# Optimization experiments

Hardware: AMD Instinct MI355X
Metric: run time of the kernel (lower is better)

The kernel has to match this reference:

```python
import jax, jax.numpy as jnp
import numpy as np

D_MODEL = 1024
NUM_HEADS = 16
D_K = D_MODEL // NUM_HEADS
NEG_INF = -1e9


def setup_inputs() -> dict:
    key = jax.random.key(0)
    ks = jax.random.split(key, 9)
    B, S, D = 4, 2048, D_MODEL
    scale = 1.0 / np.sqrt(D)
    inp = {
        "x": jax.random.normal(ks[0], (B, S, D), dtype=jnp.float32),
        "Wq": jax.random.normal(ks[1], (D, D), dtype=jnp.float32) * scale,
        "bq": jnp.zeros((D,), dtype=jnp.float32),
        "Wk": jax.random.normal(ks[2], (D, D), dtype=jnp.float32) * scale,
        "bk": jnp.zeros((D,), dtype=jnp.float32),
        "Wv": jax.random.normal(ks[3], (D, D), dtype=jnp.float32) * scale,
        "bv": jnp.zeros((D,), dtype=jnp.float32),
        "Wo": jax.random.normal(ks[4], (D, D), dtype=jnp.float32) * scale,
        "bo": jnp.zeros((D,), dtype=jnp.float32),
    }
    return inp


def reference(x, Wq, bq, Wk, bk, Wv, bv, Wo, bo):
    B, S, D = x.shape
    H, dk = NUM_HEADS, D_K
    # padding mask: token is pad if any feature == 0; shape [B,1,1,S] (keys)
    mask = (x == 0).any(axis=-1)[:, None, None, :]

    def split_heads(t):  # [B,S,D] -> [B,H,S,dk]
        return t.reshape(B, S, H, dk).transpose(0, 2, 1, 3)

    q = split_heads(x @ Wq + bq)
    k = split_heads(x @ Wk + bk)
    v = split_heads(x @ Wv + bv)

    scores = jnp.einsum("bhqd,bhkd->bhqk", q, k) / np.sqrt(dk).astype(x.dtype)
    scores = jnp.where(mask, jnp.asarray(NEG_INF, x.dtype), scores)
    weights = jax.nn.softmax(scores, axis=-1)
    context = jnp.einsum("bhqk,bhkd->bhqd", weights, v)
    context = context.transpose(0, 2, 1, 3).reshape(B, S, D)
    return context @ Wo + bo
```

## Files before the change

kernel.cpp:

```cpp
#include <hip/hip_runtime.h>
#include <cstdint>
#include <cstddef>

static constexpr int Bz = 4, S = 2048, Dm = 1024, H = 16, DK = 64;
static constexpr int M = Bz * S;

typedef __attribute__((ext_vector_type(8))) short bf16x8;
typedef __attribute__((ext_vector_type(4))) float f32x4;

__device__ __forceinline__ unsigned short f2b(float f) {
    unsigned u = __float_as_uint(f);
    return (unsigned short)((u + 0x7FFFu + ((u >> 16) & 1u)) >> 16);
}

__device__ __forceinline__ unsigned cvtpk(float lo, float hi) {
    unsigned r;
    asm("v_cvt_pk_bf16_f32 %0, %1, %2" : "=v"(r) : "v"(lo), "v"(hi));
    return r;
}

__device__ __forceinline__ void gld_lds16(const void* g, void* l) {
    __builtin_amdgcn_global_load_lds(
        (const __attribute__((address_space(1))) unsigned int*)g,
        (__attribute__((address_space(3))) unsigned int*)l, 16, 0, 0);
}

__global__ __launch_bounds__(256) void k_convx(const float* __restrict__ x,
                                               unsigned short* __restrict__ xb,
                                               unsigned char* __restrict__ mask) {
    const int row = blockIdx.x;
    const int t = threadIdx.x;
    const float4 v = *(const float4*)(x + (size_t)row * Dm + t * 4);
    const bool z = (v.x == 0.f) | (v.y == 0.f) | (v.z == 0.f) | (v.w == 0.f);
    ushort4 o;
    o.x = f2b(v.x); o.y = f2b(v.y); o.z = f2b(v.z); o.w = f2b(v.w);
    *(ushort4*)(xb + (size_t)row * Dm + t * 4) = o;
    __shared__ int zf;
    if (t == 0) zf = 0;
    __syncthreads();
    if (z) zf = 1;
    __syncthreads();
    if (t == 0) mask[row] = (unsigned char)zf;
}

__global__ __launch_bounds__(256) void k_convw(const float* __restrict__ Wq, const float* __restrict__ Wk,
                                               const float* __restrict__ Wv, const float* __restrict__ Wo,
                                               unsigned short* __restrict__ Wt) {
    const float* W = (blockIdx.z == 0) ? Wq : (blockIdx.z == 1) ? Wk : (blockIdx.z == 2) ? Wv : Wo;
    unsigned short* o = Wt + (size_t)blockIdx.z * Dm * Dm;
    __shared__ float tile[32][33];
    const int k0 = blockIdx.x * 32, n0 = blockIdx.y * 32;
    const int tx = threadIdx.x, ty = threadIdx.y;
#pragma unroll
    for (int i = 0; i < 4; i++)
        tile[ty + 8 * i][tx] = W[(size_t)(k0 + ty + 8 * i) * Dm + n0 + tx];
    __syncthreads();
#pragma unroll
    for (int i = 0; i < 4; i++)
        o[(size_t)(n0 + ty + 8 * i) * Dm + k0 + tx] = f2b(tile[tx][ty + 8 * i]);
}

template <int MODE>
__global__ __launch_bounds__(256) void k_gemm(
    const unsigned short* __restrict__ A,
    const unsigned short* __restrict__ Bw,
    const float* __restrict__ bias0, const float* __restrict__ bias1, const float* __restrict__ bias2,
    unsigned short* __restrict__ Qo, unsigned short* __restrict__ Ko,
    unsigned short* __restrict__ Vto, float* __restrict__ Co)
{
    __shared__ unsigned short sA[128 * 32];
    __shared__ unsigned short sB[128 * 32];
    const int m0 = blockIdx.x * 128;
    const int gn0 = blockIdx.y * 128;
    const int tid = threadIdx.x;
    const int lane = tid & 63;
    const int wid = tid >> 6;
    const int wm = wid & 1, wn = wid >> 1;
    const int srow = tid >> 2;
    const int sc8 = (tid & 3) * 8;
    const int lr = lane & 15;
    const int lg = lane >> 4;
    f32x4 acc[4][4] = {};
    const unsigned short* Ag = A + (size_t)(m0 + srow) * Dm + sc8;
    const unsigned short* Bg = Bw + (size_t)(gn0 + srow) * Dm + sc8;
    unsigned short* const lA = sA + wid * 512;
    unsigned short* const lB = sB + wid * 512;
    for (int k0 = 0; k0 < Dm; k0 += 32) {
        __syncthreads();
        gld_lds16(Ag + k0, lA);
        gld_lds16(Ag + (size_t)64 * Dm + k0, lA + 2048);
        gld_lds16(Bg + k0, lB);
        gld_lds16(Bg + (size_t)64 * Dm + k0, lB + 2048);
        __syncthreads();
        bf16x8 af[4], bg[4];
#pragma unroll
        for (int mi = 0; mi < 4; mi++)
            af[mi] = *(const bf16x8*)&sA[(wm * 64 + mi * 16 + lr) * 32 + lg * 8];
#pragma unroll
        for (int ni = 0; ni < 4; ni++)
            bg[ni] = *(const bf16x8*)&sB[(wn * 64 + ni * 16 + lr) * 32 + lg * 8];
#pragma unroll
        for (int mi = 0; mi < 4; mi++)
#pragma unroll
            for (int ni = 0; ni < 4; ni++)
                acc[mi][ni] = __builtin_amdgcn_mfma_f32_16x16x32_bf16(af[mi], bg[ni], acc[mi][ni], 0, 0, 0);
    }
#pragma unroll
    for (int mi = 0; mi < 4; mi++) {
        const int row0 = m0 + wm * 64 + mi * 16 + lg * 4;
#pragma unroll
        for (int ni = 0; ni < 4; ni++) {
            const int gn = gn0 + wn * 64 + ni * 16 + lr;
            const int t = gn >> 10;
            const int n = gn & 1023;
            const int h = n >> 6, d = n & 63;
            const float bsv = (MODE == 0)
                ? ((t == 0) ? bias0[n] : (t == 1) ? bias1[n] : bias2[n])
                : bias0[gn];
#pragma unroll
            for (int r = 0; r < 4; r++) {
                const int row = row0 + r;
                const float v = acc[mi][ni][r] + bsv;
                if (MODE == 0) {
                    const int bb = row >> 11;
                    const int s = row & (S - 1);
                    const size_t bh = (size_t)bb * H + h;
                    const unsigned short ub = f2b(v);
                    if (t == 0)      Qo[(bh * S + s) * DK + d] = ub;
                    else if (t == 1) Ko[(bh * S + s) * DK + d] = ub;
                    else {
                        const int k5 = s & 31;
                        const int sp = (s & ~31) | ((k5 & 12) << 1) | ((k5 >> 4) << 2) | (k5 & 3);
                        Vto[(bh * DK + d) * S + sp] = ub;
                    }
                } else {
                    Co[(size_t)row * Dm + gn] = v;
                }
            }
        }
    }
}

__global__ __launch_bounds__(512) void k_attn(
    const unsigned short* __restrict__ Q, const unsigned short* __restrict__ K,
    const unsigned short* __restrict__ Vt, const unsigned char* __restrict__ mask,
    unsigned short* __restrict__ ctx)
{
    __shared__ unsigned short sK[2 * 4096];
    __shared__ unsigned short sV[2 * 4096];
    const int wg = blockIdx.x;
    const int sz = (wg & 7) * 128 + (wg >> 3);
    const int xt = sz & 15;
    const int bh = sz >> 4;
    const int bidx = bh >> 4, h = bh & 15;
    const int tid = threadIdx.x, lane = tid & 63, wid = tid >> 6;
    const int lr = lane & 15, lg = lane >> 4;
    const int qbase = xt * 128 + wid * 16;
    const size_t hoff = (size_t)bh * S * DK;
    const bf16x8 aq0 = *(const bf16x8*)(Q + hoff + (size_t)(qbase + lr) * DK + lg * 8);
    const bf16x8 aq1 = *(const bf16x8*)(Q + hoff + (size_t)(qbase + lr) * DK + 32 + lg * 8);
    const unsigned char* mrow = mask + bidx * S;
    f32x4 o[4] = {};
    f32x4 lvec = {};
    constexpr float SCL2 = 0.125f * 1.44269504089f;
    constexpr float CSH  = 8.0f * 1.44269504089f;
    const int rsub = lane >> 3;
    const int csrc = ((lane & 7) ^ rsub) << 4;
    const char* gK = (const char*)(K + hoff) + (size_t)(wid * 8 + rsub) * (DK * 2) + csrc;
    const char* gV = (const char*)(Vt + hoff) + (size_t)(wid * 8 + rsub) * (S * 2) + csrc;
    constexpr int NT = S / 64;
    unsigned short* const dK0 = sK + wid * 512;
    unsigned short* const dV0 = sV + wid * 512;
    unsigned short* const dK1 = dK0 + 4096;
    unsigned short* const dV1 = dV0 + 4096;
    const char* const sKb0 = (const char*)sK;
    const char* const sKb1 = sKb0 + 8192;
    const char* const sVb0 = (const char*)sV;
    const char* const sVb1 = sVb0 + 8192;

    gld_lds16(gK, dK0);
    gld_lds16(gV, dV0);
    unsigned char mb = mrow[lane];
    gK += 8192; gV += 128;

    auto body = [&](int t, const char* sKc, const char* sVc,
                    unsigned short* dKn, unsigned short* dVn) {
        asm volatile("s_waitcnt vmcnt(0)" ::: "memory");
        __builtin_amdgcn_s_barrier();
        __builtin_amdgcn_sched_barrier(0);
        const unsigned char mbc = mb;
        if (t + 1 < NT) {
            gld_lds16(gK, dKn);
            gld_lds16(gV, dVn);
            mb = mrow[(t + 1) * 64 + lane];
            gK += 8192; gV += 128;
        }
        const unsigned long long bal = __ballot(mbc != 0);
        f32x4 zz[4];
        __builtin_amdgcn_s_setprio(1);
#pragma unroll
        for (int nt = 0; nt < 4; nt++) {
            const int row = nt * 16 + lr;
            const int sw = (row & 7) << 4;
            const bf16x8 kf0 = *(const bf16x8*)(sKc + ((row * 128 + lg * 16) ^ sw));
            const bf16x8 kf1 = *(const bf16x8*)(sKc + ((row * 128 + 64 + lg * 16) ^ sw));
            f32x4 a = {};
            a = __builtin_amdgcn_mfma_f32_16x16x32_bf16(kf0, aq0, a, 0, 0, 0);
            zz[nt] = __builtin_amdgcn_mfma_f32_16x16x32_bf16(kf1, aq1, a, 0, 0, 0);
        }
        __builtin_amdgcn_s_setprio(0);
        if (bal) {
#pragma unroll
            for (int nt = 0; nt < 4; nt++)
#pragma unroll
                for (int r = 0; r < 4; r++)
                    if ((bal >> (nt * 16 + lg * 4 + r)) & 1) zz[nt][r] = -1e9f;
        }
#pragma unroll
        for (int nt = 0; nt < 4; nt++) {
            zz[nt] = zz[nt] * SCL2 - CSH;
#pragma unroll
            for (int r = 0; r < 4; r++) zz[nt][r] = exp2f(zz[nt][r]);
            lvec += zz[nt];
        }
        union { unsigned u[4]; bf16x8 v; } w0, w1;
        w0.u[0] = cvtpk(zz[0][0], zz[0][1]); w0.u[1] = cvtpk(zz[0][2], zz[0][3]);
        w0.u[2] = cvtpk(zz[1][0], zz[1][1]); w0.u[3] = cvtpk(zz[1][2], zz[1][3]);
        w1.u[0] = cvtpk(zz[2][0], zz[2][1]); w1.u[1] = cvtpk(zz[2][2], zz[2][3]);
        w1.u[2] = cvtpk(zz[3][0], zz[3][1]); w1.u[3] = cvtpk(zz[3][2], zz[3][3]);
        __builtin_amdgcn_s_setprio(1);
#pragma unroll
        for (int dt = 0; dt < 4; dt++) {
            const int row = dt * 16 + lr;
            const int sw = (row & 7) << 4;
            const bf16x8 v0 = *(const bf16x8*)(sVc + ((row * 128 + lg * 16) ^ sw));
            const bf16x8 v1 = *(const bf16x8*)(sVc + ((row * 128 + 64 + lg * 16) ^ sw));
            o[dt] = __builtin_amdgcn_mfma_f32_16x16x32_bf16(w0.v, v0, o[dt], 0, 0, 0);
            o[dt] = __builtin_amdgcn_mfma_f32_16x16x32_bf16(w1.v, v1, o[dt], 0, 0, 0);
        }
        __builtin_amdgcn_s_setprio(0);
        asm volatile("s_waitcnt lgkmcnt(0)" ::: "memory");
    };

    for (int t = 0; t < NT; t += 2) {
        body(t,     sKb0, sVb0, dK1, dV1);
        body(t + 1, sKb1, sVb1, dK0, dV0);
    }

    float ls = (lvec[0] + lvec[1]) + (lvec[2] + lvec[3]);
    ls += __shfl_xor(ls, 16, 64);
    ls += __shfl_xor(ls, 32, 64);
#pragma unroll
    for (int r = 0; r < 4; r++) {
        const float lq = __shfl(ls, lg * 4 + r, 16);
        const float inv = 1.f / lq;
        const int s = qbase + lg * 4 + r;
#pragma unroll
        for (int dt = 0; dt < 4; dt++)
            ctx[((size_t)bidx * S + s) * Dm + h * 64 + dt * 16 + lr] = f2b(o[dt][r] * inv);
    }
}

extern "C" void kernel_launch(void* const* d_in, const int* in_sizes, int n_in,
                              void* d_out, int out_size, void* d_ws, size_t ws_size,
                              hipStream_t stream)
{
    (void)in_sizes; (void)n_in; (void)out_size; (void)ws_size;
    const float* x  = (const float*)d_in[0];
    const float* Wq = (const float*)d_in[1];
    const float* bq = (const float*)d_in[2];
    const float* Wk = (const float*)d_in[3];
    const float* bk = (const float*)d_in[4];
    const float* Wv = (const float*)d_in[5];
    const float* bv = (const float*)d_in[6];
    const float* Wo = (const float*)d_in[7];
    const float* bo = (const float*)d_in[8];
    float* out = (float*)d_out;
    char* ws = (char*)d_ws;
    unsigned short* xb  = (unsigned short*)(ws);
    unsigned short* Wt  = (unsigned short*)(ws + ((size_t)16 << 20));
    unsigned short* Qb  = (unsigned short*)(ws + ((size_t)24 << 20));
    unsigned short* Kb  = (unsigned short*)(ws + ((size_t)40 << 20));
    unsigned short* Vtb = (unsigned short*)(ws + ((size_t)56 << 20));
    unsigned short* ctx = (unsigned short*)(ws + ((size_t)72 << 20));
    unsigned char*  msk = (unsigned char*)(ws + ((size_t)88 << 20));

    k_convx<<<dim3(M), dim3(256), 0, stream>>>(x, xb, msk);
    k_convw<<<dim3(Dm / 32, Dm / 32, 4), dim3(32, 8), 0, stream>>>(Wq, Wk, Wv, Wo, Wt);
    k_gemm<0><<<dim3(M / 128, 3072 / 128), dim3(256), 0, stream>>>(
        xb, Wt, bq, bk, bv, Qb, Kb, Vtb, nullptr);
    k_attn<<<dim3(Bz * H * (S / 128)), dim3(512), 0, stream>>>(Qb, Kb, Vtb, msk, ctx);
    k_gemm<1><<<dim3(M / 128, 1024 / 128), dim3(256), 0, stream>>>(
        ctx, Wt + (size_t)3 * Dm * Dm, bo, nullptr, nullptr, nullptr, nullptr, nullptr, out);
}
```

Baseline: 236.7 us.

## Give each attention wave two query tiles and fold softmax scale into Q

The attention kernel moves from 8 waves each owning 16 query rows to 4 waves each owning 32 rows. Each K/V fragment read from LDS now feeds twice as many MFMAs, and each wave issues two global-to-LDS loads per tile. The softmax scale (1/8 times log2 e) is folded into the Q projection epilogue, which removes the per-score multiply and the constant shift before exp2. The cost is more accumulator registers per wave (occupancy is set through launch bounds) and dropping the stabilising shift, which leaves less margin against exp2 overflow.

```diff
diff --git a/kernel.cpp b/kernel.cpp
--- a/kernel.cpp
+++ b/kernel.cpp
@@ -125,13 +125,14 @@
                     const int bb = row >> 11;
                     const int s = row & (S - 1);
                     const size_t bh = (size_t)bb * H + h;
-                    const unsigned short ub = f2b(v);
-                    if (t == 0)      Qo[(bh * S + s) * DK + d] = ub;
-                    else if (t == 1) Ko[(bh * S + s) * DK + d] = ub;
-                    else {
+                    if (t == 0) {
+                        Qo[(bh * S + s) * DK + d] = f2b(v * 0.18033688011f);
+                    } else if (t == 1) {
+                        Ko[(bh * S + s) * DK + d] = f2b(v);
+                    } else {
                         const int k5 = s & 31;
                         const int sp = (s & ~31) | ((k5 & 12) << 1) | ((k5 >> 4) << 2) | (k5 & 3);
-                        Vto[(bh * DK + d) * S + sp] = ub;
+                        Vto[(bh * DK + d) * S + sp] = f2b(v);
                     }
                 } else {
                     Co[(size_t)row * Dm + gn] = v;
@@ -141,7 +142,7 @@
     }
 }
 
-__global__ __launch_bounds__(512) void k_attn(
+__global__ __launch_bounds__(256, 4) void k_attn(
     const unsigned short* __restrict__ Q, const unsigned short* __restrict__ K,
     const unsigned short* __restrict__ Vt, const unsigned char* __restrict__ mask,
     unsigned short* __restrict__ ctx)
@@ -155,48 +156,45 @@
     const int bidx = bh >> 4, h = bh & 15;
     const int tid = threadIdx.x, lane = tid & 63, wid = tid >> 6;
     const int lr = lane & 15, lg = lane >> 4;
-    const int qbase = xt * 128 + wid * 16;
+    const int qbase = xt * 128 + wid * 32;
     const size_t hoff = (size_t)bh * S * DK;
-    const bf16x8 aq0 = *(const bf16x8*)(Q + hoff + (size_t)(qbase + lr) * DK + lg * 8);
-    const bf16x8 aq1 = *(const bf16x8*)(Q + hoff + (size_t)(qbase + lr) * DK + 32 + lg * 8);
+    const unsigned short* qp = Q + hoff + (size_t)(qbase + lr) * DK;
+    const bf16x8 aqA0 = *(const bf16x8*)(qp + lg * 8);
+    const bf16x8 aqA1 = *(const bf16x8*)(qp + 32 + lg * 8);
+    const bf16x8 aqB0 = *(const bf16x8*)(qp + 16 * DK + lg * 8);
+    const bf16x8 aqB1 = *(const bf16x8*)(qp + 16 * DK + 32 + lg * 8);
     const unsigned char* mrow = mask + bidx * S;
-    f32x4 o[4] = {};
-    f32x4 lvec = {};
-    constexpr float SCL2 = 0.125f * 1.44269504089f;
-    constexpr float CSH  = 8.0f * 1.44269504089f;
-    const int rsub = lane >> 3;
-    const int csrc = ((lane & 7) ^ rsub) << 4;
-    const char* gK = (const char*)(K + hoff) + (size_t)(wid * 8 + rsub) * (DK * 2) + csrc;
-    const char* gV = (const char*)(Vt + hoff) + (size_t)(wid * 8 + rsub) * (S * 2) + csrc;
+    f32x4 oA[4] = {}, oB[4] = {};
+    f32x4 lvA = {}, lvB = {};
+    const int rw = lane >> 3;
+    const int row0 = wid * 16 + rw;
+    const int csrc = ((lane & 7) ^ rw) << 4;
+    const char* gK0 = (const char*)(K + hoff) + (size_t)row0 * 128 + csrc;
+    const char* gK1 = gK0 + 8 * 128;
+    const char* gV0 = (const char*)(Vt + hoff) + (size_t)row0 * (S * 2) + csrc;
+    const char* gV1 = gV0 + (size_t)8 * (S * 2);
     constexpr int NT = S / 64;
-    unsigned short* const dK0 = sK + wid * 512;
-    unsigned short* const dV0 = sV + wid * 512;
-    unsigned short* const dK1 = dK0 + 4096;
-    unsigned short* const dV1 = dV0 + 4096;
-    const char* const sKb0 = (const char*)sK;
-    const char* const sKb1 = sKb0 + 8192;
-    const char* const sVb0 = (const char*)sV;
-    const char* const sVb1 = sVb0 + 8192;
-
-    gld_lds16(gK, dK0);
-    gld_lds16(gV, dV0);
+    unsigned short* const wK = sK + wid * 1024;
+    unsigned short* const wV = sV + wid * 1024;
+
+    gld_lds16(gK0, wK);        gld_lds16(gK1, wK + 512);
+    gld_lds16(gV0, wV);        gld_lds16(gV1, wV + 512);
     unsigned char mb = mrow[lane];
-    gK += 8192; gV += 128;
-
-    auto body = [&](int t, const char* sKc, const char* sVc,
-                    unsigned short* dKn, unsigned short* dVn) {
+    gK0 += 8192; gK1 += 8192; gV0 += 128; gV1 += 128;
+
+    auto body = [&](int t, const char* sKc, const char* sVc, int nbuf) {
         asm volatile("s_waitcnt vmcnt(0)" ::: "memory");
         __builtin_amdgcn_s_barrier();
         __builtin_amdgcn_sched_barrier(0);
         const unsigned char mbc = mb;
         if (t + 1 < NT) {
-            gld_lds16(gK, dKn);
-            gld_lds16(gV, dVn);
+            gld_lds16(gK0, wK + nbuf * 4096);  gld_lds16(gK1, wK + nbuf * 4096 + 512);
+            gld_lds16(gV0, wV + nbuf * 4096);  gld_lds16(gV1, wV + nbuf * 4096 + 512);
             mb = mrow[(t + 1) * 64 + lane];
-            gK += 8192; gV += 128;
+            gK0 += 8192; gK1 += 8192; gV0 += 128; gV1 += 128;
         }
         const unsigned long long bal = __ballot(mbc != 0);
-        f32x4 zz[4];
+        f32x4 zA[4], zB[4];
         __builtin_amdgcn_s_setprio(1);
 #pragma unroll
         for (int nt = 0; nt < 4; nt++) {
@@ -205,8 +203,11 @@
             const bf16x8 kf0 = *(const bf16x8*)(sKc + ((row * 128 + lg * 16) ^ sw));
             const bf16x8 kf1 = *(const bf16x8*)(sKc + ((row * 128 + 64 + lg * 16) ^ sw));
             f32x4 a = {};
-            a = __builtin_amdgcn_mfma_f32_16x16x32_bf16(kf0, aq0, a, 0, 0, 0);
-            zz[nt] = __builtin_amdgcn_mfma_f32_16x16x32_bf16(kf1, aq1, a, 0, 0, 0);
+            a = __builtin_amdgcn_mfma_f32_16x16x32_bf16(kf0, aqA0, a, 0, 0, 0);
+            zA[nt] = __builtin_amdgcn_mfma_f32_16x16x32_bf16(kf1, aqA1, a, 0, 0, 0);
+            f32x4 b = {};
+            b = __builtin_amdgcn_mfma_f32_16x16x32_bf16(kf0, aqB0, b, 0, 0, 0);
+            zB[nt] = __builtin_amdgcn_mfma_f32_16x16x32_bf16(kf1, aqB1, b, 0, 0, 0);
         }
         __builtin_amdgcn_s_setprio(0);
         if (bal) {
@@ -214,20 +215,24 @@
             for (int nt = 0; nt < 4; nt++)
 #pragma unroll
                 for (int r = 0; r < 4; r++)
-                    if ((bal >> (nt * 16 + lg * 4 + r)) & 1) zz[nt][r] = -1e9f;
+                    if ((bal >> (nt * 16 + lg * 4 + r)) & 1) { zA[nt][r] = -1e9f; zB[nt][r] = -1e9f; }
         }
 #pragma unroll
         for (int nt = 0; nt < 4; nt++) {
-            zz[nt] = zz[nt] * SCL2 - CSH;
-#pragma unroll
-            for (int r = 0; r < 4; r++) zz[nt][r] = exp2f(zz[nt][r]);
-            lvec += zz[nt];
-        }
-        union { unsigned u[4]; bf16x8 v; } w0, w1;
-        w0.u[0] = cvtpk(zz[0][0], zz[0][1]); w0.u[1] = cvtpk(zz[0][2], zz[0][3]);
-        w0.u[2] = cvtpk(zz[1][0], zz[1][1]); w0.u[3] = cvtpk(zz[1][2], zz[1][3]);
-        w1.u[0] = cvtpk(zz[2][0], zz[2][1]); w1.u[1] = cvtpk(zz[2][2], zz[2][3]);
-        w1.u[2] = cvtpk(zz[3][0], zz[3][1]); w1.u[3] = cvtpk(zz[3][2], zz[3][3]);
+#pragma unroll
+            for (int r = 0; r < 4; r++) { zA[nt][r] = exp2f(zA[nt][r]); zB[nt][r] = exp2f(zB[nt][r]); }
+            lvA += zA[nt];
+            lvB += zB[nt];
+        }
+        union { unsigned u[4]; bf16x8 v; } wA0, wA1, wB0, wB1;
+        wA0.u[0] = cvtpk(zA[0][0], zA[0][1]); wA0.u[1] = cvtpk(zA[0][2], zA[0][3]);
+        wA0.u[2] = cvtpk(zA[1][0], zA[1][1]); wA0.u[3] = cvtpk(zA[1][2], zA[1][3]);
+        wA1.u[0] = cvtpk(zA[2][0], zA[2][1]); wA1.u[1] = cvtpk(zA[2][2], zA[2][3]);
+        wA1.u[2] = cvtpk(zA[3][0], zA[3][1]); wA1.u[3] = cvtpk(zA[3][2], zA[3][3]);
+        wB0.u[0] = cvtpk(zB[0][0], zB[0][1]); wB0.u[1] = cvtpk(zB[0][2], zB[0][3]);
+        wB0.u[2] = cvtpk(zB[1][0], zB[1][1]); wB0.u[3] = cvtpk(zB[1][2], zB[1][3]);
+        wB1.u[0] = cvtpk(zB[2][0], zB[2][1]); wB1.u[1] = cvtpk(zB[2][2], zB[2][3]);
+        wB1.u[2] = cvtpk(zB[3][0], zB[3][1]); wB1.u[3] = cvtpk(zB[3][2], zB[3][3]);
         __builtin_amdgcn_s_setprio(1);
 #pragma unroll
         for (int dt = 0; dt < 4; dt++) {
@@ -235,29 +240,41 @@
             const int sw = (row & 7) << 4;
             const bf16x8 v0 = *(const bf16x8*)(sVc + ((row * 128 + lg * 16) ^ sw));
             const bf16x8 v1 = *(const bf16x8*)(sVc + ((row * 128 + 64 + lg * 16) ^ sw));
-            o[dt] = __builtin_amdgcn_mfma_f32_16x16x32_bf16(w0.v, v0, o[dt], 0, 0, 0);
-            o[dt] = __builtin_amdgcn_mfma_f32_16x16x32_bf16(w1.v, v1, o[dt], 0, 0, 0);
+            oA[dt] = __builtin_amdgcn_mfma_f32_16x16x32_bf16(wA0.v, v0, oA[dt], 0, 0, 0);
+            oA[dt] = __builtin_amdgcn_mfma_f32_16x16x32_bf16(wA1.v, v1, oA[dt], 0, 0, 0);
+            oB[dt] = __builtin_amdgcn_mfma_f32_16x16x32_bf16(wB0.v, v0, oB[dt], 0, 0, 0);
+            oB[dt] = __builtin_amdgcn_mfma_f32_16x16x32_bf16(wB1.v, v1, oB[dt], 0, 0, 0);
         }
         __builtin_amdgcn_s_setprio(0);
         asm volatile("s_waitcnt lgkmcnt(0)" ::: "memory");
     };
 
+    const char* const sKb0 = (const char*)sK;
+    const char* const sKb1 = sKb0 + 8192;
+    const char* const sVb0 = (const char*)sV;
+    const char* const sVb1 = sVb0 + 8192;
     for (int t = 0; t < NT; t += 2) {
-        body(t,     sKb0, sVb0, dK1, dV1);
-        body(t + 1, sKb1, sVb1, dK0, dV0);
+        body(t,     sKb0, sVb0, 1);
+        body(t + 1, sKb1, sVb1, 0);
     }
 
-    float ls = (lvec[0] + lvec[1]) + (lvec[2] + lvec[3]);
-    ls += __shfl_xor(ls, 16, 64);
-    ls += __shfl_xor(ls, 32, 64);
+    float lsA = (lvA[0] + lvA[1]) + (lvA[2] + lvA[3]);
+    lsA += __shfl_xor(lsA, 16, 64);
+    lsA += __shfl_xor(lsA, 32, 64);
+    float lsB = (lvB[0] + lvB[1]) + (lvB[2] + lvB[3]);
+    lsB += __shfl_xor(lsB, 16, 64);
+    lsB += __shfl_xor(lsB, 32, 64);
 #pragma unroll
     for (int r = 0; r < 4; r++) {
-        const float lq = __shfl(ls, lg * 4 + r, 16);
-        const float inv = 1.f / lq;
-        const int s = qbase + lg * 4 + r;
-#pragma unroll
-        for (int dt = 0; dt < 4; dt++)
-            ctx[((size_t)bidx * S + s) * Dm + h * 64 + dt * 16 + lr] = f2b(o[dt][r] * inv);
+        const float iA = 1.f / __shfl(lsA, lg * 4 + r, 16);
+        const float iB = 1.f / __shfl(lsB, lg * 4 + r, 16);
+        const int sA_ = qbase + lg * 4 + r;
+#pragma unroll
+        for (int dt = 0; dt < 4; dt++) {
+            const int col = h * 64 + dt * 16 + lr;
+            ctx[((size_t)bidx * S + sA_) * Dm + col]      = f2b(oA[dt][r] * iA);
+            ctx[((size_t)bidx * S + sA_ + 16) * Dm + col] = f2b(oB[dt][r] * iB);
+        }
     }
 }
 
@@ -289,7 +306,7 @@
     k_convw<<<dim3(Dm / 32, Dm / 32, 4), dim3(32, 8), 0, stream>>>(Wq, Wk, Wv, Wo, Wt);
     k_gemm<0><<<dim3(M / 128, 3072 / 128), dim3(256), 0, stream>>>(
         xb, Wt, bq, bk, bv, Qb, Kb, Vtb, nullptr);
-    k_attn<<<dim3(Bz * H * (S / 128)), dim3(512), 0, stream>>>(Qb, Kb, Vtb, msk, ctx);
+    k_attn<<<dim3(Bz * H * (S / 128)), dim3(256), 0, stream>>>(Qb, Kb, Vtb, msk, ctx);
     k_gemm<1><<<dim3(M / 128, 1024 / 128), dim3(256), 0, stream>>>(
         ctx, Wt + (size_t)3 * Dm * Dm, bo, nullptr, nullptr, nullptr, nullptr, nullptr, out);
 }
```

Result: slower. 337.7 us (+42.7%).
